# Optimization experiments

Measured on AMD Instinct MI355X. Metric: run time of the kernel, lower is better.

The kernel has to match this reference:

```python
import jax, jax.numpy as jnp
import numpy as np

B, S, H = 2, 4096, 1024  # batch, seq_len, hidden_size (= all_head_size)


def setup_inputs() -> dict:
    key = jax.random.key(0)
    ks = jax.random.split(key, 7)
    sc = 1.0 / np.sqrt(H)
    return {
        "hidden_states": jax.random.normal(ks[0], (B, S, H), dtype=jnp.float32),
        "Wq": jax.random.normal(ks[1], (H, H), dtype=jnp.float32) * sc,
        "bq": jnp.zeros((H,), dtype=jnp.float32),
        "Wk": jax.random.normal(ks[2], (H, H), dtype=jnp.float32) * sc,
        "bk": jnp.zeros((H,), dtype=jnp.float32),
        "Wv": jax.random.normal(ks[3], (H, H), dtype=jnp.float32) * sc,
        "bv": jnp.zeros((H,), dtype=jnp.float32),
    }


def reference(hidden_states, Wq, bq, Wk, bk, Wv, bv):
    # QKV projections (weights stored as [in, out] = W.T of torch Linear)
    q = hidden_states @ Wq + bq  # [B,S,H]
    k = hidden_states @ Wk + bk
    v = hidden_states @ Wv + bv
    # Raw attention: no head split, no 1/sqrt(d) scaling (faithful to source)
    scores = jnp.einsum("bqh,bkh->bqk", q, k)  # [B,S,S]
    probs = jax.nn.softmax(scores, axis=-1)
    context = jnp.einsum("bqk,bkh->bqh", probs, v)  # [B,S,H]
    return context
```

## Files before the change

### kernel.cpp

```cpp
#include <hip/hip_runtime.h>
#include <stdint.h>

typedef __attribute__((ext_vector_type(8))) short short8;
typedef __attribute__((ext_vector_type(8))) _Float16 half8;
typedef __attribute__((ext_vector_type(4))) float f32x4;

__device__ __forceinline__ unsigned short f2h(float x) {
  _Float16 h = (_Float16)x;
  return __builtin_bit_cast(unsigned short, h);
}
__device__ __forceinline__ float h2f(unsigned short u) {
  return (float)__builtin_bit_cast(_Float16, u);
}

#define GLOAD16(gsrc, ldst)                                              \
  __builtin_amdgcn_global_load_lds(                                      \
      (const __attribute__((address_space(1))) void*)(gsrc),             \
      (__attribute__((address_space(3))) void*)(ldst), 16, 0, 0)

#define VM(N) asm volatile("s_waitcnt vmcnt(" #N ")" ::: "memory")
#define BARSYNC __builtin_amdgcn_s_barrier()
#define LGKM0                                                \
  do {                                                       \
    asm volatile("s_waitcnt lgkmcnt(0)" ::: "memory");       \
    __builtin_amdgcn_sched_barrier(0);                       \
  } while (0)

__global__ __launch_bounds__(256) void split_pair_f16_kernel(
    const float* __restrict__ in, unsigned short* __restrict__ h,
    unsigned short* __restrict__ l) {
  size_t i = (size_t)blockIdx.x * 256 + threadIdx.x;
  float4 a = ((const float4*)in)[2 * i];
  float4 b = ((const float4*)in)[2 * i + 1];
  ushort4 h0 = make_ushort4(f2h(a.x), f2h(a.y), f2h(a.z), f2h(a.w));
  ushort4 h1 = make_ushort4(f2h(b.x), f2h(b.y), f2h(b.z), f2h(b.w));
  ((ushort4*)h)[2 * i] = h0;
  ((ushort4*)h)[2 * i + 1] = h1;
  ((ushort4*)l)[2 * i] = make_ushort4(
      f2h(a.x - h2f(h0.x)), f2h(a.y - h2f(h0.y)),
      f2h(a.z - h2f(h0.z)), f2h(a.w - h2f(h0.w)));
  ((ushort4*)l)[2 * i + 1] = make_ushort4(
      f2h(b.x - h2f(h1.x)), f2h(b.y - h2f(h1.y)),
      f2h(b.z - h2f(h1.z)), f2h(b.w - h2f(h1.w)));
}

__global__ __launch_bounds__(256) void transpose_f16_kernel(
    const float* __restrict__ W, unsigned short* __restrict__ hT,
    int Kd, int Nd) {
  __shared__ float tile[32][33];
  int r = threadIdx.x >> 3;
  int c = (threadIdx.x & 7) * 4;
  int k0 = blockIdx.y * 32, n0 = blockIdx.x * 32;
  float4 v = *(const float4*)&W[(size_t)(k0 + r) * Nd + n0 + c];
  tile[r][c] = v.x; tile[r][c + 1] = v.y; tile[r][c + 2] = v.z; tile[r][c + 3] = v.w;
  __syncthreads();
  size_t o = (size_t)(n0 + r) * Kd + k0 + c;
  *(ushort4*)&hT[o] = make_ushort4(f2h(tile[c + 0][r]), f2h(tile[c + 1][r]),
                                   f2h(tile[c + 2][r]), f2h(tile[c + 3][r]));
}

__global__ __launch_bounds__(256) void transpose_v_kernel(
    const unsigned short* __restrict__ Vs, unsigned short* __restrict__ vT) {
  __shared__ unsigned short tile[32][36];
  int r = threadIdx.x >> 3;
  int c = (threadIdx.x & 7) * 4;
  int col0 = blockIdx.x * 32;
  int row0 = blockIdx.y * 32;
  ushort4 v = *(const ushort4*)&Vs[(size_t)(row0 + r) * 1024 + col0 + c];
  tile[r][c] = v.x; tile[r][c + 1] = v.y; tile[r][c + 2] = v.z; tile[r][c + 3] = v.w;
  __syncthreads();
  ushort4 o = make_ushort4(tile[c + 0][r], tile[c + 1][r],
                           tile[c + 2][r], tile[c + 3][r]);
  *(ushort4*)&vT[(size_t)(col0 + r) * 8192 + row0 + c] = o;
}

__global__ __launch_bounds__(512, 4) void qkv_kernel(
    const unsigned short* __restrict__ Ah, const unsigned short* __restrict__ Al,
    const unsigned short* __restrict__ WT, const float* __restrict__ bq,
    const float* __restrict__ bk, const float* __restrict__ bv,
    unsigned short* __restrict__ qh, unsigned short* __restrict__ kh,
    unsigned short* __restrict__ vS) {
  __shared__ __align__(16) char smem[2 * 40 * 1024];
  constexpr int lda = 1024, ldb = 1024, K = 1024;
  const int t = threadIdx.x, wid = t >> 6, lane = t & 63;
  const int waveM = wid >> 2, waveN = wid & 3;
  const int lr0 = lane & 15, lk0 = (lane >> 4) * 8;
  const int m0 = blockIdx.y * 256, n0 = blockIdx.x * 128;

  const unsigned short* slot_src[5];
#pragma unroll
  for (int s = 0; s < 5; ++s) {
    int si = 5 * wid + s;
    const unsigned short* p;
    if (si < 16)      p = Ah + (size_t)(m0 + si * 16 + lr0) * lda + lk0;
    else if (si < 32) p = Al + (size_t)(m0 + (si - 16) * 16 + lr0) * lda + lk0;
    else              p = WT + (size_t)(n0 + (si - 32) * 16 + lr0) * ldb + lk0;
    slot_src[s] = p;
  }

  const int NTILES = K >> 5;
  f32x4 acc[8][2] = {};

#pragma unroll
  for (int s = 0; s < 5; ++s)
    GLOAD16(slot_src[s], smem + (5 * wid + s) * 1024);
  VM(0);
  BARSYNC;
  __builtin_amdgcn_sched_barrier(0);

  for (int tile = 0; tile < NTILES; ++tile) {
    const char* cb = smem + (tile & 1) * 40960;
    char* nb = smem + ((tile + 1) & 1) * 40960;
    if (tile + 1 < NTILES) {
#pragma unroll
      for (int s = 0; s < 5; ++s)
        GLOAD16(slot_src[s] + (size_t)(tile + 1) * 32,
                nb + (5 * wid + s) * 1024);
    }
    half8 bf[2];
#pragma unroll
    for (int p = 0; p < 4; ++p) {
      half8 ahf[2], alf[2];
#pragma unroll
      for (int i = 0; i < 2; ++i) {
        int mg = waveM * 8 + 2 * p + i;
        ahf[i] = *(const half8*)(cb + mg * 1024 + lane * 16);
        alf[i] = *(const half8*)(cb + (16 + mg) * 1024 + lane * 16);
      }
      if (p == 0) {
#pragma unroll
        for (int j = 0; j < 2; ++j) {
          int ng = waveN * 2 + j;
          bf[j] = *(const half8*)(cb + (32 + ng) * 1024 + lane * 16);
        }
      }
      __builtin_amdgcn_s_setprio(1);
#pragma unroll
      for (int i = 0; i < 2; ++i)
#pragma unroll
        for (int j = 0; j < 2; ++j) {
          f32x4 c = acc[2 * p + i][j];
          c = __builtin_amdgcn_mfma_f32_16x16x32_f16(ahf[i], bf[j], c, 0, 0, 0);
          c = __builtin_amdgcn_mfma_f32_16x16x32_f16(alf[i], bf[j], c, 0, 0, 0);
          acc[2 * p + i][j] = c;
        }
      __builtin_amdgcn_s_setprio(0);
    }
    if (tile + 1 < NTILES) {
      LGKM0;
      VM(0);
      BARSYNC;
      __builtin_amdgcn_sched_barrier(0);
    }
  }

  const int or0 = (lane >> 4) * 4;
  const int slab = n0 >> 10;
#pragma unroll
  for (int mm = 0; mm < 8; ++mm)
#pragma unroll
    for (int j = 0; j < 2; ++j)
#pragma unroll
      for (int r = 0; r < 4; ++r) {
        int row = m0 + waveM * 128 + mm * 16 + or0 + r;
        int col = (n0 & 1023) + waveN * 32 + j * 16 + lr0;
        float x = acc[mm][j][r];
        if (slab == 0) {
          qh[(size_t)row * 1024 + col] = f2h(x + bq[col]);
        } else if (slab == 1) {
          kh[(size_t)row * 1024 + col] = f2h(x + bk[col]);
        } else {
          vS[(size_t)row * 1024 + col] = f2h(x + bv[col]);
        }
      }
}

__global__ __launch_bounds__(512, 2) void g1q_kernel(
    const unsigned short* __restrict__ Abase, size_t Astr, int lda,
    const unsigned short* __restrict__ Bbase, size_t Bstr, int ldb,
    float* __restrict__ outF, size_t Ostr, int ldo, int K) {
  __shared__ __align__(16) char smem[3 * 32 * 1024];
  const int t = threadIdx.x, wid = t >> 6, lane = t & 63;
  const int waveM = wid >> 2, waveN = wid & 3;
  const int lr0 = lane & 15, lk0 = (lane >> 4) * 8;
  const int m0 = blockIdx.y * 256, n0 = blockIdx.x * 256;
  const unsigned short* A = Abase + (size_t)blockIdx.z * Astr;
  const unsigned short* B = Bbase + (size_t)blockIdx.z * Bstr;
  float* out = outF + (size_t)blockIdx.z * Ostr;

  const unsigned short* slot_src[4];
#pragma unroll
  for (int s = 0; s < 4; ++s) {
    int si = 4 * wid + s;
    const unsigned short* p;
    if (si < 16) p = A + (size_t)(m0 + si * 16 + lr0) * lda + lk0;
    else         p = B + (size_t)(n0 + (si - 16) * 16 + lr0) * ldb + lk0;
    slot_src[s] = p;
  }

  const int NTILES = K >> 5;
  f32x4 acc[8][4] = {};

#pragma unroll
  for (int tt = 0; tt < 2; ++tt)
#pragma unroll
    for (int s = 0; s < 4; ++s)
      GLOAD16(slot_src[s] + (size_t)tt * 32,
              smem + tt * 32768 + (4 * wid + s) * 1024);
  VM(4);
  BARSYNC;
  __builtin_amdgcn_sched_barrier(0);

  for (int tile = 0; tile < NTILES; ++tile) {
    const int cur = tile % 3, nxt = (tile + 2) % 3;
    const bool do_stage = (tile + 2) < NTILES;
    const char* cb = smem + cur * 32768;
    char* nb = smem + nxt * 32768;
    half8 bf[4];
#pragma unroll
    for (int p = 0; p < 4; ++p) {
      half8 af[2];
#pragma unroll
      for (int i = 0; i < 2; ++i) {
        int mg = waveM * 8 + 2 * p + i;
        af[i] = *(const half8*)(cb + mg * 1024 + lane * 16);
      }
      if (p == 0) {
#pragma unroll
        for (int j = 0; j < 4; ++j) {
          int ng = waveN * 4 + j;
          bf[j] = *(const half8*)(cb + 16384 + ng * 1024 + lane * 16);
        }
      }
      if (do_stage)
        GLOAD16(slot_src[p] + (size_t)(tile + 2) * 32,
                nb + (4 * wid + p) * 1024);
      __builtin_amdgcn_s_setprio(1);
#pragma unroll
      for (int i = 0; i < 2; ++i)
#pragma unroll
        for (int j = 0; j < 4; ++j)
          acc[2 * p + i][j] = __builtin_amdgcn_mfma_f32_16x16x32_f16(
              af[i], bf[j], acc[2 * p + i][j], 0, 0, 0);
      __builtin_amdgcn_s_setprio(0);
    }
    if (tile + 1 < NTILES) {
      LGKM0;
      if (do_stage) VM(4); else VM(0);
      BARSYNC;
      __builtin_amdgcn_sched_barrier(0);
    }
  }

  const int or0 = (lane >> 4) * 4;
#pragma unroll
  for (int mm = 0; mm < 8; ++mm)
#pragma unroll
    for (int j = 0; j < 4; ++j)
#pragma unroll
      for (int r = 0; r < 4; ++r)
        out[(size_t)(m0 + waveM * 128 + mm * 16 + or0 + r) * ldo +
            (n0 + waveN * 64 + j * 16 + lr0)] = acc[mm][j][r];
}

__global__ __launch_bounds__(512, 2) void g1_kernel(
    const unsigned short* __restrict__ Abase, size_t Astr, int lda,
    const unsigned short* __restrict__ Bbase, size_t Bstr, int ldb,
    float* __restrict__ outF, size_t Ostr, int ldo, int K) {
  __shared__ __align__(16) char smem[3 * 48 * 1024];
  const int t = threadIdx.x, wid = t >> 6, lane = t & 63;
  const int waveM = wid >> 2, waveN = wid & 3;
  const int lr0 = lane & 15, lk0 = (lane >> 4) * 8;
  const int m0 = blockIdx.y * 256, n0 = blockIdx.x * 128;
  const unsigned short* A = Abase + (size_t)blockIdx.z * Astr;
  const unsigned short* B = Bbase + (size_t)blockIdx.z * Bstr;
  float* out = outF + (size_t)blockIdx.z * Ostr;

  const unsigned short* slot_src[6];
#pragma unroll
  for (int s = 0; s < 6; ++s) {
    int si = 6 * wid + s;
    const unsigned short* p;
    if (si < 16)      p = A + (size_t)(m0 + si * 16 + lr0) * lda + lk0;
    else if (si < 32) p = A + (size_t)(m0 + (si - 16) * 16 + lr0) * lda + 32 + lk0;
    else if (si < 40) p = B + (size_t)(n0 + (si - 32) * 16 + lr0) * ldb + lk0;
    else              p = B + (size_t)(n0 + (si - 40) * 16 + lr0) * ldb + 32 + lk0;
    slot_src[s] = p;
  }

  const int NTILES = K >> 6;
  f32x4 acc[8][2] = {};

#pragma unroll
  for (int tt = 0; tt < 2; ++tt)
#pragma unroll
    for (int s = 0; s < 6; ++s)
      GLOAD16(slot_src[s] + (size_t)tt * 64,
              smem + tt * 49152 + (6 * wid + s) * 1024);
  VM(6);
  BARSYNC;
  __builtin_amdgcn_sched_barrier(0);

  for (int tile = 0; tile < NTILES; ++tile) {
    const int cur = tile % 3, nxt = (tile + 2) % 3;
    const bool do_stage = (tile + 2) < NTILES;
    const char* cb = smem + cur * 49152;
    char* nb = smem + nxt * 49152;
    half8 blo[2], bhi[2];
#pragma unroll
    for (int p = 0; p < 4; ++p) {
      half8 alo[2], ahi[2];
#pragma unroll
      for (int i = 0; i < 2; ++i) {
        int mg = waveM * 8 + 2 * p + i;
        alo[i] = *(const half8*)(cb + mg * 1024 + lane * 16);
        ahi[i] = *(const half8*)(cb + (16 + mg) * 1024 + lane * 16);
      }
      if (p == 0) {
#pragma unroll
        for (int j = 0; j < 2; ++j) {
          int ng = waveN * 2 + j;
          blo[j] = *(const half8*)(cb + (32 + ng) * 1024 + lane * 16);
          bhi[j] = *(const half8*)(cb + (40 + ng) * 1024 + lane * 16);
        }
      }
      if (do_stage && p < 3) {
#pragma unroll
        for (int s = 0; s < 2; ++s) {
          int slot = 2 * p + s;
          GLOAD16(slot_src[slot] + (size_t)(tile + 2) * 64,
                  nb + (6 * wid + slot) * 1024);
        }
      }
      __builtin_amdgcn_s_setprio(1);
#pragma unroll
      for (int i = 0; i < 2; ++i)
#pragma unroll
        for (int j = 0; j < 2; ++j) {
          f32x4 c = acc[2 * p + i][j];
          c = __builtin_amdgcn_mfma_f32_16x16x32_f16(alo[i], blo[j], c, 0, 0, 0);
          c = __builtin_amdgcn_mfma_f32_16x16x32_f16(ahi[i], bhi[j], c, 0, 0, 0);
          acc[2 * p + i][j] = c;
        }
      __builtin_amdgcn_s_setprio(0);
    }
    if (tile + 1 < NTILES) {
      LGKM0;
      if (do_stage) VM(6); else VM(0);
      BARSYNC;
      __builtin_amdgcn_sched_barrier(0);
    }
  }

  const int or0 = (lane >> 4) * 4;
#pragma unroll
  for (int mm = 0; mm < 8; ++mm)
#pragma unroll
    for (int j = 0; j < 2; ++j)
#pragma unroll
      for (int r = 0; r < 4; ++r)
        out[(size_t)(m0 + waveM * 128 + mm * 16 + or0 + r) * ldo +
            (n0 + waveN * 32 + j * 16 + lr0)] = acc[mm][j][r];
}

__global__ __launch_bounds__(256) void softmax_rows_kernel(
    const float* Sm, unsigned short* P, int ncol, int pld) {
  const int t = threadIdx.x;
  const float* srow = Sm + (size_t)blockIdx.x * ncol;
  float4 v[4];
  float m = -3.4e38f;
#pragma unroll
  for (int i = 0; i < 4; ++i) {
    v[i] = ((const float4*)srow)[t + 256 * i];
    m = fmaxf(m, fmaxf(fmaxf(v[i].x, v[i].y), fmaxf(v[i].z, v[i].w)));
  }
#pragma unroll
  for (int off = 32; off >= 1; off >>= 1) m = fmaxf(m, __shfl_down(m, off));
  __shared__ float redm[4];
  if ((t & 63) == 0) redm[t >> 6] = m;
  __syncthreads();
  m = fmaxf(fmaxf(redm[0], redm[1]), fmaxf(redm[2], redm[3]));
  float s = 0.f;
#pragma unroll
  for (int i = 0; i < 4; ++i) {
    v[i].x = __expf(v[i].x - m);
    v[i].y = __expf(v[i].y - m);
    v[i].z = __expf(v[i].z - m);
    v[i].w = __expf(v[i].w - m);
    s += v[i].x + v[i].y + v[i].z + v[i].w;
  }
#pragma unroll
  for (int off = 32; off >= 1; off >>= 1) s += __shfl_down(s, off);
  __shared__ float reds[4];
  if ((t & 63) == 0) reds[t >> 6] = s;
  __syncthreads();
  s = reds[0] + reds[1] + reds[2] + reds[3];
  float inv = 1.f / s;
  unsigned short* prow = P + (size_t)blockIdx.x * pld;
#pragma unroll
  for (int i = 0; i < 4; ++i) {
    ushort4 o = make_ushort4(f2h(v[i].x * inv), f2h(v[i].y * inv),
                             f2h(v[i].z * inv), f2h(v[i].w * inv));
    ((ushort4*)prow)[t + 256 * i] = o;
  }
}

extern "C" void kernel_launch(void* const* d_in, const int* in_sizes, int n_in,
                              void* d_out, int out_size, void* d_ws, size_t ws_size,
                              hipStream_t stream) {
  const float* hs = (const float*)d_in[0];
  const float* Wq = (const float*)d_in[1];
  const float* bq = (const float*)d_in[2];
  const float* Wk = (const float*)d_in[3];
  const float* bk = (const float*)d_in[4];
  const float* Wv = (const float*)d_in[5];
  const float* bv = (const float*)d_in[6];
  float* out = (float*)d_out;

  constexpr int Ss = 4096, Hh = 1024;
  constexpr int Mm = 8192;
  constexpr size_t TOK = (size_t)Ss * Hh;
  char* ws = (char*)d_ws;
  const size_t MB = 1024 * 1024;

  unsigned short* qh = (unsigned short*)(ws + 0 * MB);
  unsigned short* kh = (unsigned short*)(ws + 16 * MB);
  unsigned short* vT = (unsigned short*)(ws + 32 * MB);
  char* rb = ws + 48 * MB;
  unsigned short* hs_h = (unsigned short*)(rb + 0 * MB);
  unsigned short* hs_l = (unsigned short*)(rb + 16 * MB);
  unsigned short* WT = (unsigned short*)(rb + 32 * MB);
  unsigned short* vS = (unsigned short*)(rb + 38 * MB);
  float* Sf = (float*)rb;

  const bool big = ws_size >= (size_t)176 * MB;

  split_pair_f16_kernel<<<dim3(Mm * Hh / 2048), 256, 0, stream>>>(hs, hs_h, hs_l);
  transpose_f16_kernel<<<dim3(32, 32), 256, 0, stream>>>(Wq, WT, Hh, Hh);
  transpose_f16_kernel<<<dim3(32, 32), 256, 0, stream>>>(
      Wk, WT + (size_t)1024 * 1024, Hh, Hh);
  transpose_f16_kernel<<<dim3(32, 32), 256, 0, stream>>>(
      Wv, WT + (size_t)2048 * 1024, Hh, Hh);

  qkv_kernel<<<dim3(24, 32), 512, 0, stream>>>(
      hs_h, hs_l, WT, bq, bk, bv, qh, kh, vS);

  transpose_v_kernel<<<dim3(32, 256), 256, 0, stream>>>(vS, vT);

  if (big) {
    g1q_kernel<<<dim3(16, 16, 2), 512, 0, stream>>>(
        qh, TOK, Hh, kh, TOK, Hh, Sf, (size_t)Ss * Ss, Ss, Hh);
    softmax_rows_kernel<<<dim3(2 * Ss), 256, 0, stream>>>(
        Sf, (unsigned short*)Sf, Ss, 2 * Ss);
    g1_kernel<<<dim3(8, 16, 2), 512, 0, stream>>>(
        (const unsigned short*)Sf, (size_t)Ss * 2 * Ss, 2 * Ss,
        vT, (size_t)Ss, Mm, out, TOK, Hh, Ss);
  } else {
    float* Sb = (float*)rb;
    unsigned short* Pb = (unsigned short*)(rb + 64 * MB);
    for (int b = 0; b < 2; ++b) {
      g1q_kernel<<<dim3(16, 16, 1), 512, 0, stream>>>(
          qh + b * TOK, 0, Hh, kh + b * TOK, 0, Hh, Sb, 0, Ss, Hh);
      softmax_rows_kernel<<<dim3(Ss), 256, 0, stream>>>(Sb, Pb, Ss, Ss);
      g1_kernel<<<dim3(8, 16, 1), 512, 0, stream>>>(
          Pb, 0, Ss, vT + (size_t)b * Ss, 0, Mm, out + b * TOK, 0, Hh, Ss);
    }
  }
}
```

Baseline: 392.1 us.

## Rewrite QK^T GEMM with K=64 tiles and 8-phase interleaved load/MFMA schedule

Replaces the QK^T score GEMM kernel with a variant that stages 64-wide K tiles into two 64KB LDS buffers. Each K tile is split into four quadrant MFMA phases that alternate with partial global-to-LDS loads, separated by barriers, in the style of an 8-wave ping-pong schedule. The aim is better overlap of global loads, LDS reads and MFMA work, and fewer main-loop iterations. In exchange it uses 128KB of LDS per block, which likely limits occupancy to one block per CU despite launch bounds of 2, and adds many more barriers.

```diff
diff --git a/kernel.cpp b/kernel.cpp
--- a/kernel.cpp
+++ b/kernel.cpp
@@ -175,11 +175,42 @@
       }
 }
 
-__global__ __launch_bounds__(512, 2) void g1q_kernel(
+#define ST8(h, T, bufb)                                                   \
+  do {                                                                    \
+    const unsigned short* _s = ssrc[h] + (size_t)(T) * 64;                \
+    char* _d = smem + (bufb) * 65536 + sdst[h];                           \
+    GLOAD16(_s, _d);                                                      \
+    GLOAD16(_s + 32, _d + 1024);                                          \
+  } while (0)
+
+#define RDA(bufb, qr)                                                     \
+  _Pragma("unroll") for (int _i = 0; _i < 4; ++_i)                        \
+  _Pragma("unroll") for (int _kk = 0; _kk < 2; ++_kk)                     \
+      areg[_i][_kk] = *(const half8*)(smem + (bufb) * 65536 +             \
+          ((waveM * 8 + (qr) * 4 + _i) * 2 + _kk) * 1024 + lane * 16);
+
+#define RDB(bufb, qc)                                                     \
+  _Pragma("unroll") for (int _j = 0; _j < 2; ++_j)                        \
+  _Pragma("unroll") for (int _kk = 0; _kk < 2; ++_kk)                     \
+      breg[_j][_kk] = *(const half8*)(smem + (bufb) * 65536 + 32768 +     \
+          ((waveN * 4 + (qc) * 2 + _j) * 2 + _kk) * 1024 + lane * 16);
+
+#define MM16(qr, qc)                                                      \
+  __builtin_amdgcn_s_setprio(1);                                          \
+  _Pragma("unroll") for (int _i = 0; _i < 4; ++_i)                        \
+  _Pragma("unroll") for (int _j = 0; _j < 2; ++_j)                        \
+  _Pragma("unroll") for (int _kk = 0; _kk < 2; ++_kk)                     \
+      acc[(qr) * 4 + _i][(qc) * 2 + _j] =                                 \
+          __builtin_amdgcn_mfma_f32_16x16x32_f16(                         \
+              areg[_i][_kk], breg[_j][_kk],                               \
+              acc[(qr) * 4 + _i][(qc) * 2 + _j], 0, 0, 0);                \
+  __builtin_amdgcn_s_setprio(0);
+
+__global__ __launch_bounds__(512, 2) void g8q_kernel(
     const unsigned short* __restrict__ Abase, size_t Astr, int lda,
     const unsigned short* __restrict__ Bbase, size_t Bstr, int ldb,
     float* __restrict__ outF, size_t Ostr, int ldo, int K) {
-  __shared__ __align__(16) char smem[3 * 32 * 1024];
+  __shared__ __align__(16) char smem[131072];
   const int t = threadIdx.x, wid = t >> 6, lane = t & 63;
   const int waveM = wid >> 2, waveN = wid & 3;
   const int lr0 = lane & 15, lk0 = (lane >> 4) * 8;
@@ -188,79 +219,75 @@
   const unsigned short* B = Bbase + (size_t)blockIdx.z * Bstr;
   float* out = outF + (size_t)blockIdx.z * Ostr;
 
-  const unsigned short* slot_src[4];
-#pragma unroll
-  for (int s = 0; s < 4; ++s) {
-    int si = 4 * wid + s;
-    const unsigned short* p;
-    if (si < 16) p = A + (size_t)(m0 + si * 16 + lr0) * lda + lk0;
-    else         p = B + (size_t)(n0 + (si - 16) * 16 + lr0) * ldb + lk0;
-    slot_src[s] = p;
-  }
-
-  const int NTILES = K >> 5;
+  const int rgA0 = (wid & 3) + ((wid >> 2) << 3);
+  const int rgA1 = rgA0 + 4;
+  const int cgB0 = (wid & 1) + ((wid >> 1) << 2);
+  const int cgB1 = cgB0 + 2;
+  const unsigned short* ssrc[4];
+  int sdst[4];
+  ssrc[0] = A + (size_t)(m0 + rgA0 * 16 + lr0) * lda + lk0;
+  ssrc[1] = A + (size_t)(m0 + rgA1 * 16 + lr0) * lda + lk0;
+  ssrc[2] = B + (size_t)(n0 + cgB0 * 16 + lr0) * ldb + lk0;
+  ssrc[3] = B + (size_t)(n0 + cgB1 * 16 + lr0) * ldb + lk0;
+  sdst[0] = (rgA0 * 2) * 1024;
+  sdst[1] = (rgA1 * 2) * 1024;
+  sdst[2] = 32768 + (cgB0 * 2) * 1024;
+  sdst[3] = 32768 + (cgB1 * 2) * 1024;
+
+  const int NT = K >> 6, NT2 = NT >> 1;
   f32x4 acc[8][4] = {};
-
-#pragma unroll
-  for (int tt = 0; tt < 2; ++tt)
-#pragma unroll
-    for (int s = 0; s < 4; ++s)
-      GLOAD16(slot_src[s] + (size_t)tt * 32,
-              smem + tt * 32768 + (4 * wid + s) * 1024);
-  VM(4);
+  half8 areg[4][2], breg[2][2];
+
+  ST8(0, 0, 0); ST8(2, 0, 0); ST8(1, 0, 0); ST8(3, 0, 0);
+  ST8(2, 1, 1); ST8(1, 1, 1); ST8(3, 1, 1);
+  VM(6);
   BARSYNC;
   __builtin_amdgcn_sched_barrier(0);
 
-  for (int tile = 0; tile < NTILES; ++tile) {
-    const int cur = tile % 3, nxt = (tile + 2) % 3;
-    const bool do_stage = (tile + 2) < NTILES;
-    const char* cb = smem + cur * 32768;
-    char* nb = smem + nxt * 32768;
-    half8 bf[4];
-#pragma unroll
-    for (int p = 0; p < 4; ++p) {
-      half8 af[2];
-#pragma unroll
-      for (int i = 0; i < 2; ++i) {
-        int mg = waveM * 8 + 2 * p + i;
-        af[i] = *(const half8*)(cb + mg * 1024 + lane * 16);
-      }
-      if (p == 0) {
-#pragma unroll
-        for (int j = 0; j < 4; ++j) {
-          int ng = waveN * 4 + j;
-          bf[j] = *(const half8*)(cb + 16384 + ng * 1024 + lane * 16);
-        }
-      }
-      if (do_stage)
-        GLOAD16(slot_src[p] + (size_t)(tile + 2) * 32,
-                nb + (4 * wid + p) * 1024);
-      __builtin_amdgcn_s_setprio(1);
-#pragma unroll
-      for (int i = 0; i < 2; ++i)
-#pragma unroll
-        for (int j = 0; j < 4; ++j)
-          acc[2 * p + i][j] = __builtin_amdgcn_mfma_f32_16x16x32_f16(
-              af[i], bf[j], acc[2 * p + i][j], 0, 0, 0);
-      __builtin_amdgcn_s_setprio(0);
-    }
-    if (tile + 1 < NTILES) {
-      LGKM0;
-      if (do_stage) VM(4); else VM(0);
-      BARSYNC;
-      __builtin_amdgcn_sched_barrier(0);
-    }
+#pragma unroll 1
+  for (int it = 0; it < NT2; ++it) {
+    const int tt = 2 * it;
+    const bool s2 = (tt + 2) < NT;
+    const bool s3 = (tt + 3) < NT;
+    RDA(0, 0) RDB(0, 0)
+    ST8(0, tt + 1, 1);
+    BARSYNC; LGKM0; MM16(0, 0) BARSYNC;
+    RDA(0, 1)
+    if (s2) ST8(2, tt + 2, 0);
+    BARSYNC; LGKM0; MM16(1, 0) BARSYNC;
+    RDB(0, 1)
+    if (s2) ST8(1, tt + 2, 0);
+    BARSYNC; LGKM0; MM16(1, 1) BARSYNC;
+    RDA(0, 0)
+    if (s2) ST8(3, tt + 2, 0);
+    BARSYNC; LGKM0; MM16(0, 1)
+    if (s2) { VM(6); } else { VM(0); }
+    BARSYNC;
+    RDA(1, 0) RDB(1, 0)
+    if (s2) ST8(0, tt + 2, 0);
+    BARSYNC; LGKM0; MM16(0, 0) BARSYNC;
+    RDA(1, 1)
+    if (s3) ST8(2, tt + 3, 1);
+    BARSYNC; LGKM0; MM16(1, 0) BARSYNC;
+    RDB(1, 1)
+    if (s3) ST8(1, tt + 3, 1);
+    BARSYNC; LGKM0; MM16(1, 1) BARSYNC;
+    RDA(1, 0)
+    if (s3) ST8(3, tt + 3, 1);
+    BARSYNC; LGKM0; MM16(0, 1)
+    if (s3) { VM(6); }
+    BARSYNC;
   }
 
   const int or0 = (lane >> 4) * 4;
 #pragma unroll
   for (int mm = 0; mm < 8; ++mm)
 #pragma unroll
-    for (int j = 0; j < 4; ++j)
+    for (int cg = 0; cg < 4; ++cg)
 #pragma unroll
       for (int r = 0; r < 4; ++r)
         out[(size_t)(m0 + waveM * 128 + mm * 16 + or0 + r) * ldo +
-            (n0 + waveN * 64 + j * 16 + lr0)] = acc[mm][j][r];
+            (n0 + waveN * 64 + cg * 16 + lr0)] = acc[mm][cg][r];
 }
 
 __global__ __launch_bounds__(512, 2) void g1_kernel(
@@ -448,7 +475,7 @@
   transpose_v_kernel<<<dim3(32, 256), 256, 0, stream>>>(vS, vT);
 
   if (big) {
-    g1q_kernel<<<dim3(16, 16, 2), 512, 0, stream>>>(
+    g8q_kernel<<<dim3(16, 16, 2), 512, 0, stream>>>(
         qh, TOK, Hh, kh, TOK, Hh, Sf, (size_t)Ss * Ss, Ss, Hh);
     softmax_rows_kernel<<<dim3(2 * Ss), 256, 0, stream>>>(
         Sf, (unsigned short*)Sf, Ss, 2 * Ss);
@@ -459,7 +486,7 @@
     float* Sb = (float*)rb;
     unsigned short* Pb = (unsigned short*)(rb + 64 * MB);
     for (int b = 0; b < 2; ++b) {
-      g1q_kernel<<<dim3(16, 16, 1), 512, 0, stream>>>(
+      g8q_kernel<<<dim3(16, 16, 1), 512, 0, stream>>>(
           qh + b * TOK, 0, Hh, kh + b * TOK, 0, Hh, Sb, 0, Ss, Hh);
       softmax_rows_kernel<<<dim3(Ss), 256, 0, stream>>>(Sb, Pb, Ss, Ss);
       g1_kernel<<<dim3(8, 16, 1), 512, 0, stream>>>(
```

Result: faster. 383.1 us (-2.3%).
